# Kernel tuning notes

Hardware: AMD Instinct MI355X
Metric: run time of the kernel (lower is better)

The kernel has to match this reference:

```python
import jax, jax.numpy as jnp
import numpy as np

N_BATCH = 8192   # rows/cols of score matrix
N_NEG = 16       # negatives per row (init kwarg n)
VOCAB = 100000   # item id range for sel_out


def setup_inputs() -> dict:
    key = jax.random.key(0)
    k1, k2 = jax.random.split(key)
    x = jax.random.normal(k1, (N_BATCH, N_BATCH), dtype=jnp.float32)
    sel_out = jax.random.randint(k2, (N_BATCH,), 0, VOCAB, dtype=jnp.int32)
    return {"x": x, "sel_out": sel_out}


def reference(x, sel_out):
    # mask[i, j] = 1 where item j differs from row i's target item
    mask = (sel_out[None, :] != sel_out[:, None]).astype(x.dtype)  # (n, n)
    # positive term: diagonal holds each row's target score
    pos = -jnp.mean(jax.nn.log_sigmoid(jnp.diagonal(x)))
    # top-N_NEG highest masked scores per row -> negative sample indices
    _, idx = jax.lax.top_k(x * mask, N_NEG)          # idx: (n, N_NEG)
    neg_vals = jnp.take_along_axis(x, idx, axis=1)   # gather raw scores
    # log(1 - sigmoid(v)) == log_sigmoid(-v) (numerically stable form)
    neg = -jnp.mean(jax.nn.log_sigmoid(-neg_vals))
    return pos + neg
```

## Files before the change

### kernel.cpp

```cpp
#include <hip/hip_runtime.h>
#include <math.h>

#define N_ROWS 8192
#define N_NEG 16
#define NBLK (N_ROWS / 8)
#define NEG_INF (-3.0e38f)
#define TAU0 2.5f

typedef float  f4 __attribute__((ext_vector_type(4)));
typedef int    i4 __attribute__((ext_vector_type(4)));

__device__ __forceinline__ float log_sigmoid(float v) {
    return fminf(v, 0.0f) - log1pf(__expf(-fabsf(v)));
}

__device__ __forceinline__ float bcast_lane(float v, int src) {
    return __int_as_float(__builtin_amdgcn_readlane(__float_as_int(v), src));
}

#define INSERT(mv)                                                          \
    {                                                                       \
        unsigned long long ball = __ballot((mv) > tau);                     \
        while (ball) {                                                      \
            const int src = (int)__ffsll(ball) - 1;                         \
            ball &= ball - 1;                                               \
            const float cand = bcast_lane((mv), src);                       \
            if (cand > tau) {                                               \
                float tprev = __shfl_up(t, 1);                              \
                if (lane == 0) tprev = 3.0e38f;                             \
                t = (t >= cand) ? t : (tprev >= cand ? cand : tprev);       \
                tau = fmaxf(bcast_lane(t, 15), TAU0);                       \
            }                                                               \
        }                                                                   \
    }

__global__ __launch_bounds__(512) void nsl_topk_kernel(
        const float* __restrict__ x,
        const int*   __restrict__ sel,
        float*       __restrict__ ws) {
    __shared__ float partial[8];

    const int lane = threadIdx.x & 63;
    const int wid  = threadIdx.x >> 6;
    const int row  = (blockIdx.x << 3) + wid;

    const int    seli = sel[row];
    const float* xrow = x + (size_t)row * N_ROWS;
    const float* pw   = xrow + (lane << 2);
    const i4*    ps   = reinterpret_cast<const i4*>(sel) + lane;

    float t   = NEG_INF;
    float tau = TAU0;

#define LOADB(c) __builtin_nontemporal_load(                            \
        reinterpret_cast<const f4*>(pw + ((c) << 8)))
#define CONSUME(c, PF)                                                  \
    {                                                                   \
        const f4 v = buf[(c) & 3];                                      \
        if (PF) buf[(c) & 3] = LOADB((c) + 4);                          \
        const float mxv = fmaxf(fmaxf(v[0], v[1]), fmaxf(v[2], v[3]));  \
        \
        if (__any(mxv > tau)) {                                         \
            const i4 s = ps[(c) << 6];           \
            const float m0 = (s[0] != seli) ? v[0] : 0.0f;              \
            const float m1 = (s[1] != seli) ? v[1] : 0.0f;              \
            const float m2 = (s[2] != seli) ? v[2] : 0.0f;              \
            const float m3 = (s[3] != seli) ? v[3] : 0.0f;              \
            INSERT(m0);                                                 \
            INSERT(m1);                                                 \
            INSERT(m2);                                                 \
            INSERT(m3);                                                 \
        }                                                               \
    }

    f4 buf[4];
#pragma unroll
    for (int j = 0; j < 4; ++j) buf[j] = LOADB(j);

#pragma unroll 1
    for (int g = 0; g < 7; ++g) {
        const int c = g << 2;
        CONSUME(c + 0, true);
        CONSUME(c + 1, true);
        CONSUME(c + 2, true);
        CONSUME(c + 3, true);
    }
    CONSUME(28, false);
    CONSUME(29, false);
    CONSUME(30, false);
    CONSUME(31, false);
#undef CONSUME

    float negsum;
    if (tau > TAU0) {
        float ls = (lane < 16) ? log_sigmoid(-t) : 0.0f;
        ls += __shfl_xor(ls, 8);
        ls += __shfl_xor(ls, 4);
        ls += __shfl_xor(ls, 2);
        ls += __shfl_xor(ls, 1);
        negsum = ls;
    } else {
        float dt = NEG_INF, dtau = NEG_INF;
#pragma unroll 1
        for (int c = 0; c < 32; ++c) {
            const f4 v = LOADB(c);
            const i4 s = ps[c << 6];
            float m[4];
            m[0] = (s[0] != seli) ? v[0] : 0.0f;
            m[1] = (s[1] != seli) ? v[1] : 0.0f;
            m[2] = (s[2] != seli) ? v[2] : 0.0f;
            m[3] = (s[3] != seli) ? v[3] : 0.0f;
#pragma unroll
            for (int k = 0; k < 4; ++k) {
                unsigned long long ball = __ballot(m[k] > dtau);
                while (ball) {
                    const int src = (int)__ffsll(ball) - 1;
                    const float cand = __shfl(m[k], src);
                    ball &= ball - 1;
                    if (cand > dtau) {
                        float tprev = __shfl_up(dt, 1);
                        if (lane == 0) tprev = 3.0e38f;
                        dt = (dt >= cand) ? dt : (tprev >= cand ? cand : tprev);
                        dtau = __shfl(dt, 15);
                        ball &= __ballot(m[k] > dtau);
                    }
                }
            }
        }
        float ls = (lane < 16) ? log_sigmoid(-dt) : 0.0f;
        ls += __shfl_xor(ls, 8);
        ls += __shfl_xor(ls, 4);
        ls += __shfl_xor(ls, 2);
        ls += __shfl_xor(ls, 1);
        negsum = ls;
    }
#undef LOADB

    if (lane == 0) {
        const float d = xrow[row];
        partial[wid] = -log_sigmoid(d) * (1.0f / (float)N_ROWS)
                       - negsum * (1.0f / ((float)N_ROWS * (float)N_NEG));
    }
    __syncthreads();

    if (threadIdx.x == 0) {
        float s = 0.0f;
#pragma unroll
        for (int w = 0; w < 8; ++w) s += partial[w];
        ws[blockIdx.x] = s;
    }
}

__global__ __launch_bounds__(256) void nsl_reduce_kernel(
        const float* __restrict__ ws, float* __restrict__ out) {
    __shared__ float red[4];
    float s = 0.0f;
#pragma unroll
    for (int k = 0; k < NBLK / 256; ++k) s += ws[k * 256 + threadIdx.x];
    s += __shfl_xor(s, 32);
    s += __shfl_xor(s, 16);
    s += __shfl_xor(s, 8);
    s += __shfl_xor(s, 4);
    s += __shfl_xor(s, 2);
    s += __shfl_xor(s, 1);
    const int lane = threadIdx.x & 63, wid = threadIdx.x >> 6;
    if (lane == 0) red[wid] = s;
    __syncthreads();
    if (threadIdx.x == 0)
        out[0] = red[0] + red[1] + red[2] + red[3];
}

extern "C" void kernel_launch(void* const* d_in, const int* in_sizes, int n_in,
                              void* d_out, int out_size, void* d_ws, size_t ws_size,
                              hipStream_t stream) {
    const float* x   = (const float*)d_in[0];
    const int*   sel = (const int*)d_in[1];
    float* out = (float*)d_out;
    float* ws  = (float*)d_ws;

    nsl_topk_kernel<<<dim3(NBLK), dim3(512), 0, stream>>>(x, sel, ws);
    nsl_reduce_kernel<<<dim3(1), dim3(256), 0, stream>>>(ws, out);
}
```

Before: 56.92 us.

## Queue above-threshold candidates in shared memory, defer masking and top-k insertion

Result: slower. 60.37 us (+6.1%).

```diff
diff --git a/kernel.cpp b/kernel.cpp
--- a/kernel.cpp
+++ b/kernel.cpp
@@ -6,9 +6,9 @@
 #define NBLK (N_ROWS / 8)
 #define NEG_INF (-3.0e38f)
 #define TAU0 2.5f
+#define QCAP 192
 
 typedef float  f4 __attribute__((ext_vector_type(4)));
-typedef int    i4 __attribute__((ext_vector_type(4)));
 
 __device__ __forceinline__ float log_sigmoid(float v) {
     return fminf(v, 0.0f) - log1pf(__expf(-fabsf(v)));
@@ -38,19 +38,19 @@
         const float* __restrict__ x,
         const int*   __restrict__ sel,
         float*       __restrict__ ws) {
+    __shared__ int2  q[8][QCAP];
     __shared__ float partial[8];
 
     const int lane = threadIdx.x & 63;
     const int wid  = threadIdx.x >> 6;
     const int row  = (blockIdx.x << 3) + wid;
 
-    const int    seli = sel[row];
     const float* xrow = x + (size_t)row * N_ROWS;
     const float* pw   = xrow + (lane << 2);
-    const i4*    ps   = reinterpret_cast<const i4*>(sel) + lane;
-
-    float t   = NEG_INF;
-    float tau = TAU0;
+    const unsigned long long ltmask = (1ull << lane) - 1ull;
+
+    unsigned qn = 0;
+    bool overflow = false;
 
 #define LOADB(c) __builtin_nontemporal_load(                            \
         reinterpret_cast<const f4*>(pw + ((c) << 8)))
@@ -59,17 +59,25 @@
         const f4 v = buf[(c) & 3];                                      \
         if (PF) buf[(c) & 3] = LOADB((c) + 4);                          \
         const float mxv = fmaxf(fmaxf(v[0], v[1]), fmaxf(v[2], v[3]));  \
-        \
-        if (__any(mxv > tau)) {                                         \
-            const i4 s = ps[(c) << 6];           \
-            const float m0 = (s[0] != seli) ? v[0] : 0.0f;              \
-            const float m1 = (s[1] != seli) ? v[1] : 0.0f;              \
-            const float m2 = (s[2] != seli) ? v[2] : 0.0f;              \
-            const float m3 = (s[3] != seli) ? v[3] : 0.0f;              \
-            INSERT(m0);                                                 \
-            INSERT(m1);                                                 \
-            INSERT(m2);                                                 \
-            INSERT(m3);                                                 \
+        if (__any(mxv > TAU0)) {                                        \
+            if (qn + 64 > QCAP) {                                       \
+                overflow = true;                                        \
+            } else {                                                    \
+                _Pragma("unroll")                                       \
+                for (int k = 0; k < 4; ++k) {                           \
+                    const bool hit = v[k] > TAU0;                       \
+                    const unsigned long long ball = __ballot(hit);      \
+                    if (ball) {                                         \
+                        if (hit) {                                      \
+                            const int pre = __popcll(ball & ltmask);    \
+                            q[wid][qn + pre] = make_int2(               \
+                                __float_as_int(v[k]),                   \
+                                ((c) << 8) + (lane << 2) + k);          \
+                        }                                               \
+                        qn += (unsigned)__popcll(ball);                 \
+                    }                                                   \
+                }                                                       \
+            }                                                           \
         }                                                               \
     }
 
@@ -91,8 +99,21 @@
     CONSUME(31, false);
 #undef CONSUME
 
+    const int seli = sel[row];
+    float t   = NEG_INF;
+    float tau = TAU0;
+
+    for (unsigned base = 0; base < qn; base += 64) {
+        const bool act = (base + lane) < qn;
+        const int2 e = q[wid][act ? (base + lane) : 0];
+        const int  col = act ? e.y : row;
+        const float mv = (act && sel[col] != seli) ? __int_as_float(e.x)
+                                                   : 0.0f;
+        INSERT(mv);
+    }
+
     float negsum;
-    if (tau > TAU0) {
+    if (!overflow && tau > TAU0) {
         float ls = (lane < 16) ? log_sigmoid(-t) : 0.0f;
         ls += __shfl_xor(ls, 8);
         ls += __shfl_xor(ls, 4);
@@ -104,12 +125,12 @@
 #pragma unroll 1
         for (int c = 0; c < 32; ++c) {
             const f4 v = LOADB(c);
-            const i4 s = ps[c << 6];
             float m[4];
-            m[0] = (s[0] != seli) ? v[0] : 0.0f;
-            m[1] = (s[1] != seli) ? v[1] : 0.0f;
-            m[2] = (s[2] != seli) ? v[2] : 0.0f;
-            m[3] = (s[3] != seli) ? v[3] : 0.0f;
+#pragma unroll
+            for (int k = 0; k < 4; ++k) {
+                const int col = (c << 8) + (lane << 2) + k;
+                m[k] = (sel[col] != seli) ? v[k] : 0.0f;
+            }
 #pragma unroll
             for (int k = 0; k < 4; ++k) {
                 unsigned long long ball = __ballot(m[k] > dtau);
```
